# Performance work log

Measured on AMD Instinct MI355X. Metric: run time of the kernel, lower is better.

Reference implementation:

```python
import jax, jax.numpy as jnp
import numpy as np

DIM = 32
ED = DIM * DIM          # 1024
HID = ED * 4            # 4096
EPS = 1e-5


def _ln(x, g, b):
    # LayerNorm over last two dims (d, d)
    m = x.mean(axis=(-2, -1), keepdims=True)
    v = jnp.var(x, axis=(-2, -1), keepdims=True)
    return (x - m) * jax.lax.rsqrt(v + EPS) * g + b


def setup_inputs() -> dict:
    key = jax.random.key(0)
    ks = jax.random.split(key, 10)
    b, s, d = 2, 1024, DIM
    inp = {
        "x": jax.random.normal(ks[0], (b, s, d, d), dtype=jnp.float32),
        # StateSpaceLayer params
        "log_A": jax.random.normal(ks[1], (d,), dtype=jnp.float32) * 0.02,
        "w_dt": jax.random.normal(ks[2], (d,), dtype=jnp.float32) / np.sqrt(d),
        "b_dt": jnp.zeros((), dtype=jnp.float32),
        "g_ssm": jnp.ones((d, d), dtype=jnp.float32),
        "b_ssm": jnp.zeros((d, d), dtype=jnp.float32),
        # FFN params
        "g_ffn": jnp.ones((d, d), dtype=jnp.float32),
        "b_ffn": jnp.zeros((d, d), dtype=jnp.float32),
        "W1": jax.random.normal(ks[3], (ED, HID), dtype=jnp.float32) / np.sqrt(ED),
        "bb1": jnp.zeros((HID,), dtype=jnp.float32),
        "W2": jax.random.normal(ks[4], (HID, ED), dtype=jnp.float32) / np.sqrt(HID),
        "bb2": jnp.zeros((ED,), dtype=jnp.float32),
    }
    return inp


def reference(x, log_A, w_dt, b_dt, g_ssm, b_ssm, g_ffn, b_ffn, W1, bb1, W2, bb2):
    b, s, d, _ = x.shape
    # ---- StateSpaceLayer (parallel / training path) ----
    xn = _ln(x, g_ssm, b_ssm)                          # (b,s,d,d)
    A_cont = -jnp.exp(log_A)                           # (d,)
    # dt_proj: Linear(d,1) over last axis, then squeeze -> (b,s,d)
    dt = jax.nn.softplus(jnp.einsum('bsrc,c->bsr', xn, w_dt) + b_dt)
    log_a = dt * A_cont                                # (b,s,d)
    cs = jnp.cumsum(log_a, axis=1)                     # (b,s,d)
    log_M = cs[:, :, None, :] - cs[:, None, :, :]      # (b,t,j,d)
    tmask = jnp.arange(s)[:, None] >= jnp.arange(s)[None, :]  # (t,j) causal
    M = jnp.where(tmask[None, :, :, None], jnp.exp(log_M), 0.0)
    ssm_out = jnp.einsum('btjr,bjrc->btrc', M, xn) + x  # residual
    # ---- MatrixFeedForward ----
    fn = _ln(ssm_out, g_ffn, b_ffn).reshape(b, s, d * d)
    h = jax.nn.gelu(fn @ W1 + bb1, approximate=False)
    y = (h @ W2 + bb2).reshape(b, s, d, d)
    return ssm_out + y
```

## Files before the change

kernel.cpp:

```cpp
#include <hip/hip_runtime.h>
#include <math.h>

#define EPSF 1e-5f

typedef __attribute__((ext_vector_type(4))) float f32x4;
typedef __attribute__((ext_vector_type(4))) int i32x4;
typedef __attribute__((ext_vector_type(8))) int i32x8;

__device__ __forceinline__ unsigned short f2bf(float f) {
  unsigned int u = __float_as_uint(f);
  u += 0x7FFFu + ((u >> 16) & 1u);
  return (unsigned short)(u >> 16);
}
__device__ __forceinline__ float bf2f(unsigned short u) {
  return __uint_as_float((unsigned int)u << 16);
}

__device__ __forceinline__ void async_load16(const void* g, void* l) {
  __builtin_amdgcn_global_load_lds(
      (const __attribute__((address_space(1))) void*)g,
      (__attribute__((address_space(3))) void*)l, 16, 0, 0);
}


__global__ __launch_bounds__(256) void k_pre(
    const float* __restrict__ x, const float* __restrict__ g, const float* __restrict__ bta,
    const float* __restrict__ w_dt, const float* __restrict__ b_dt,
    const float* __restrict__ log_A, unsigned short* __restrict__ xn, float* __restrict__ log_a,
    const float* __restrict__ W1, unsigned char* __restrict__ W1t,
    const float* __restrict__ W2, unsigned char* __restrict__ W2t) {
  __shared__ float smem[64 * 65];
  int tid = threadIdx.x;
  if (blockIdx.x < 2048) {
    int bs = blockIdx.x;
    int t = tid;
    float4 v = ((const float4*)(x + (size_t)bs * 1024))[t];
    float s = v.x + v.y + v.z + v.w;
    float ss = v.x * v.x + v.y * v.y + v.z * v.z + v.w * v.w;
    #pragma unroll
    for (int o = 1; o < 64; o <<= 1) { s += __shfl_xor(s, o); ss += __shfl_xor(ss, o); }
    float* red = smem;
    int w = t >> 6;
    if ((t & 63) == 0) { red[w] = s; red[4 + w] = ss; }
    __syncthreads();
    float S = red[0] + red[1] + red[2] + red[3];
    float SS = red[4] + red[5] + red[6] + red[7];
    float m = S * (1.0f / 1024.0f);
    float var = SS * (1.0f / 1024.0f) - m * m;
    float inv = rsqrtf(var + EPSF);
    float4 gv = ((const float4*)g)[t];
    float4 bv = ((const float4*)bta)[t];
    float4 o;
    o.x = (v.x - m) * inv * gv.x + bv.x;
    o.y = (v.y - m) * inv * gv.y + bv.y;
    o.z = (v.z - m) * inv * gv.z + bv.z;
    o.w = (v.w - m) * inv * gv.w + bv.w;
    ushort4 ob;
    ob.x = f2bf(o.x); ob.y = f2bf(o.y); ob.z = f2bf(o.z); ob.w = f2bf(o.w);
    ((ushort4*)(xn + (size_t)bs * 1024))[t] = ob;
    float4 wv = ((const float4*)w_dt)[t & 7];
    float part = o.x * wv.x + o.y * wv.y + o.z * wv.z + o.w * wv.w;
    part += __shfl_xor(part, 1);
    part += __shfl_xor(part, 2);
    part += __shfl_xor(part, 4);
    if ((t & 7) == 0) {
      int r = t >> 3;
      float z = part + b_dt[0];
      float sp = (z > 20.0f) ? z : log1pf(expf(z));
      log_a[(size_t)bs * 32 + r] = sp * (-expf(log_A[r]));
    }
  } else {
    int bid = blockIdx.x - 2048;
    bool isW1 = bid < 1024;
    const float* src; unsigned char* dst; int C, r0, c0, NK;
    if (isW1) { src = W1; dst = W1t; C = 4096; NK = 8;
                c0 = (bid & 63) * 64; r0 = (bid >> 6) * 64; }
    else { bid -= 1024; src = W2; dst = W2t; C = 1024; NK = 32;
           c0 = (bid & 15) * 64; r0 = (bid >> 4) * 64; }
    #pragma unroll
    for (int q = 0; q < 4; ++q) {
      int lin = q * 256 + tid;
      int r = lin >> 4, cq = lin & 15;
      float4 v = *(const float4*)(src + (size_t)(r0 + r) * C + c0 + cq * 4);
      smem[r * 65 + cq * 4 + 0] = v.x; smem[r * 65 + cq * 4 + 1] = v.y;
      smem[r * 65 + cq * 4 + 2] = v.z; smem[r * 65 + cq * 4 + 3] = v.w;
    }
    __syncthreads();
    int c = tid & 63, kg = tid >> 6;
    int n = c0 + c;
    int k0 = r0 + kg * 16;
    int pk[4];
    #pragma unroll
    for (int q = 0; q < 4; ++q) {
      int p = __builtin_amdgcn_cvt_pk_fp8_f32(
          smem[(kg * 16 + q * 4 + 0) * 65 + c] * 16.0f,
          smem[(kg * 16 + q * 4 + 1) * 65 + c] * 16.0f, 0, false);
      pk[q] = __builtin_amdgcn_cvt_pk_fp8_f32(
          smem[(kg * 16 + q * 4 + 2) * 65 + c] * 16.0f,
          smem[(kg * 16 + q * 4 + 3) * 65 + c] * 16.0f, p, true);
    }
    size_t sb = (size_t)(n >> 4) * NK + (k0 >> 7);
    int l = ((k0 >> 5) & 3) * 16 + (n & 15);
    int4 o4; o4.x = pk[0]; o4.y = pk[1]; o4.z = pk[2]; o4.w = pk[3];
    *(int4*)(dst + sb * 2048 + ((k0 >> 4) & 1) * 1024 + l * 16) = o4;
  }
}

template <int PASS>
__global__ __launch_bounds__(256) void k_scan_pass(
    const unsigned short* __restrict__ xn, const float* __restrict__ x,
    const float* __restrict__ loga, float4* __restrict__ E, float* __restrict__ P,
    const float* __restrict__ bb2, float* __restrict__ out) {
  int bx = blockIdx.x;
  int b = bx >> 8, r = (bx >> 3) & 31, ch = bx & 7;
  int tid = threadIdx.x, cg = tid & 7, sub = tid >> 3;
  __shared__ float dec[128];
  __shared__ float4 sE[32][8];
  __shared__ float sP[32];
  if (tid < 128)
    dec[tid] = expf(loga[(size_t)(b * 1024 + ch * 128 + tid) * 32 + r]);
  __syncthreads();
  int t0 = ch * 128 + sub * 4;
  size_t base = ((size_t)(b * 1024 + t0) * 1024 + r * 32 + cg * 4) >> 2;
  const ushort4* xn4 = (const ushort4*)xn;
  float4 xv[4];
  #pragma unroll
  for (int i = 0; i < 4; ++i) {
    ushort4 u = xn4[base + (size_t)i * 256];
    xv[i].x = bf2f(u.x); xv[i].y = bf2f(u.y); xv[i].z = bf2f(u.z); xv[i].w = bf2f(u.w);
  }
  float4 S = {0.f, 0.f, 0.f, 0.f};
  float Pl = 1.0f;
  #pragma unroll
  for (int i = 0; i < 4; ++i) {
    float d = dec[sub * 4 + i];
    S.x = d * S.x + xv[i].x; S.y = d * S.y + xv[i].y;
    S.z = d * S.z + xv[i].z; S.w = d * S.w + xv[i].w;
    Pl *= d;
  }
  sE[sub][cg] = S;
  if (cg == 0) sP[sub] = Pl;
  __syncthreads();
  if (PASS == 0) {
    if (tid < 8) {
      float4 Et = {0.f, 0.f, 0.f, 0.f};
      float PP = 1.0f;
      #pragma unroll
      for (int h = 0; h < 32; ++h) {
        float p = sP[h]; float4 e = sE[h][tid];
        Et.x = p * Et.x + e.x; Et.y = p * Et.y + e.y;
        Et.z = p * Et.z + e.z; Et.w = p * Et.w + e.w;
        PP *= p;
      }
      E[((size_t)(b * 32 + r) * 8 + ch) * 8 + tid] = Et;
      if (tid == 0) P[(b * 32 + r) * 8 + ch] = PP;
    }
  } else {
    float4 Sin = {0.f, 0.f, 0.f, 0.f};
    const float4* Eb = E + (size_t)(b * 32 + r) * 64 + cg;
    const float* Pb = P + (size_t)(b * 32 + r) * 8;
    for (int h = 0; h < ch; ++h) {
      float p = Pb[h]; float4 e = Eb[h * 8];
      Sin.x = p * Sin.x + e.x; Sin.y = p * Sin.y + e.y;
      Sin.z = p * Sin.z + e.z; Sin.w = p * Sin.w + e.w;
    }
    for (int h = 0; h < sub; ++h) {
      float p = sP[h]; float4 e = sE[h][cg];
      Sin.x = p * Sin.x + e.x; Sin.y = p * Sin.y + e.y;
      Sin.z = p * Sin.z + e.z; Sin.w = p * Sin.w + e.w;
    }
    float4 bb = ((const float4*)bb2)[r * 8 + cg];
    const float4* x4 = (const float4*)x;
    float4* out4 = (float4*)out;
    #pragma unroll
    for (int i = 0; i < 4; ++i) {
      float d = dec[sub * 4 + i];
      Sin.x = d * Sin.x + xv[i].x; Sin.y = d * Sin.y + xv[i].y;
      Sin.z = d * Sin.z + xv[i].z; Sin.w = d * Sin.w + xv[i].w;
      float4 rx = x4[base + (size_t)i * 256];
      float4 oi;
      oi.x = Sin.x + rx.x + bb.x; oi.y = Sin.y + rx.y + bb.y;
      oi.z = Sin.z + rx.z + bb.z; oi.w = Sin.w + rx.w + bb.w;
      out4[base + (size_t)i * 256] = oi;
    }
  }
}

__global__ __launch_bounds__(256) void k_ln2(
    const float* __restrict__ out, const float* __restrict__ bb2,
    const float* __restrict__ g, const float* __restrict__ bta,
    unsigned char* __restrict__ fn) {
  __shared__ __align__(16) unsigned char sC[16384];
  int tid = threadIdx.x;
  int t15 = tid >> 4;
  int kc = tid & 15;
  int tok = (blockIdx.x << 4) + t15;
  const float4* row = (const float4*)(out + (size_t)tok * 1024);
  const float4* b4 = (const float4*)bb2;
  float4 v[16];
  float s = 0.f, ss = 0.f;
  #pragma unroll
  for (int ci = 0; ci < 4; ++ci) {
    int cc = kc + ci * 16;
    #pragma unroll
    for (int q = 0; q < 4; ++q) {
      float4 xv = row[cc * 4 + q];
      float4 bb = b4[cc * 4 + q];
      xv.x -= bb.x; xv.y -= bb.y; xv.z -= bb.z; xv.w -= bb.w;
      v[ci * 4 + q] = xv;
      s += xv.x + xv.y + xv.z + xv.w;
      ss += xv.x * xv.x + xv.y * xv.y + xv.z * xv.z + xv.w * xv.w;
    }
  }
  #pragma unroll
  for (int o = 1; o < 16; o <<= 1) { s += __shfl_xor(s, o); ss += __shfl_xor(ss, o); }
  float m = s * (1.0f / 1024.0f);
  float var = ss * (1.0f / 1024.0f) - m * m;
  float inv = rsqrtf(var + EPSF);
  #pragma unroll
  for (int ci = 0; ci < 4; ++ci) {
    int cc = kc + ci * 16;
    int pk[4];
    #pragma unroll
    for (int q = 0; q < 4; ++q) {
      float4 gv = ((const float4*)g)[cc * 4 + q];
      float4 bv = ((const float4*)bta)[cc * 4 + q];
      float4 xv = v[ci * 4 + q];
      float f0 = (xv.x - m) * inv * gv.x + bv.x;
      float f1 = (xv.y - m) * inv * gv.y + bv.y;
      float f2 = (xv.z - m) * inv * gv.z + bv.z;
      float f3 = (xv.w - m) * inv * gv.w + bv.w;
      int p = __builtin_amdgcn_cvt_pk_fp8_f32(f0, f1, 0, false);
      pk[q] = __builtin_amdgcn_cvt_pk_fp8_f32(f2, f3, p, true);
    }
    int loc = (cc >> 3) * 2048 + (cc & 1) * 1024 + (((cc >> 1) & 3) * 16 + t15) * 16;
    loc ^= ((loc >> 8) & 7) << 4;
    int4 o4; o4.x = pk[0]; o4.y = pk[1]; o4.z = pk[2]; o4.w = pk[3];
    *(int4*)(sC + loc) = o4;
  }
  __syncthreads();
  unsigned char* dst = fn + (size_t)blockIdx.x * 16384;
  #pragma unroll
  for (int p = 0; p < 4; ++p) {
    int a = (p * 256 + tid) * 16;
    int sa = a ^ (((a >> 8) & 7) << 4);
    *(int4*)(dst + a) = *(const int4*)(sC + sa);
  }
}

__global__ __launch_bounds__(256, 2) void k_gemm1(
    const unsigned char* __restrict__ Ap, const unsigned char* __restrict__ Bp,
    const float* __restrict__ bias, unsigned char* __restrict__ C8) {
  __shared__ __align__(16) unsigned char sAB[65536];
  int L = blockIdx.x;
  int xcd = L & 7;
  int nq = xcd & 3, mh = xcd >> 2;
  int rest = L >> 3;
  int nx = rest & 7, my = rest >> 3;
  int n0 = (nq * 8 + nx) * 128;
  int m0 = (mh * 8 + my) * 128;
  int tid = threadIdx.x;
  int wave = tid >> 6, lane = tid & 63;
  int wr = wave >> 1, wc = wave & 1;
  int l15 = lane & 15, quad = lane >> 4;

  f32x4 zero = {0.0f, 0.0f, 0.0f, 0.0f};
  f32x4 acc[4][4];
  #pragma unroll
  for (int i = 0; i < 4; ++i)
    #pragma unroll
    for (int j = 0; j < 4; ++j) acc[i][j] = zero;

  const unsigned char* gsrc = (wave < 2) ? Ap : Bp;
  int rt0 = (wave < 2) ? (m0 >> 4) : (n0 >> 4);
  int aoff = (wave < 2) ? 0 : 16384;
  int w01 = wave & 1;

  #pragma unroll
  for (int t = 0; t < 8; ++t) {
    int idx = w01 * 8 + t, rt = idx >> 1, h = idx & 1;
    async_load16(gsrc + ((size_t)(rt0 + rt) * 8 + 0) * 2048 + h * 1024 + lane * 16,
                 sAB + aoff + rt * 2048 + h * 1024 + lane * 16);
  }

  #pragma unroll 1
  for (int st = 0; st < 8; ++st) {
    int cur = (st & 1) * 32768;
    if (st < 7) {
      int nxt = cur ^ 32768;
      #pragma unroll
      for (int t = 0; t < 8; ++t) {
        int idx = w01 * 8 + t, rt = idx >> 1, h = idx & 1;
        async_load16(gsrc + ((size_t)(rt0 + rt) * 8 + st + 1) * 2048 + h * 1024 + lane * 16,
                     sAB + nxt + aoff + rt * 2048 + h * 1024 + lane * 16);
      }
      asm volatile("s_waitcnt vmcnt(8)" ::: "memory");
    } else {
      asm volatile("s_waitcnt vmcnt(0)" ::: "memory");
    }
    __builtin_amdgcn_s_barrier();
    const unsigned char* sA = sAB + cur;
    const unsigned char* sB = sAB + cur + 16384;
    i32x8 af[4], bf[4];
    #pragma unroll
    for (int i = 0; i < 4; ++i) {
      const unsigned char* pa = sA + (wr * 4 + i) * 2048 + lane * 16;
      i32x4 lo = *(const i32x4*)pa;
      i32x4 hi = *(const i32x4*)(pa + 1024);
      af[i] = __builtin_shufflevector(lo, hi, 0, 1, 2, 3, 4, 5, 6, 7);
    }
    #pragma unroll
    for (int j = 0; j < 4; ++j) {
      const unsigned char* pb = sB + (wc * 4 + j) * 2048 + lane * 16;
      i32x4 lo = *(const i32x4*)pb;
      i32x4 hi = *(const i32x4*)(pb + 1024);
      bf[j] = __builtin_shufflevector(lo, hi, 0, 1, 2, 3, 4, 5, 6, 7);
    }
    #pragma unroll
    for (int i = 0; i < 4; ++i)
      #pragma unroll
      for (int j = 0; j < 4; ++j)
        acc[i][j] = __builtin_amdgcn_mfma_scale_f32_16x16x128_f8f6f4(
            af[i], bf[j], acc[i][j], 0, 0, 0, 0x7F7F7F7F, 0, 0x7F7F7F7F);
    asm volatile("s_waitcnt lgkmcnt(0)" ::: "memory");
    __builtin_amdgcn_s_barrier();
  }

  unsigned char* sC = sAB;
  #pragma unroll
  for (int i = 0; i < 4; ++i) {
    #pragma unroll
    for (int j = 0; j < 4; ++j) {
      int col_l = wc * 64 + j * 16 + l15;
      float bval = bias[n0 + col_l];
      int half2 = (col_l >> 4) & 1, lb = (col_l >> 5) & 3;
      unsigned char* ld = sC + (wr * 4 + i) * 2048 + half2 * 1024 +
                          (lb * 16 + quad * 4) * 16 + l15;
      float vv[4];
      #pragma unroll
      for (int v = 0; v < 4; ++v) {
        float val = acc[i][j][v] * 0.0625f + bval;
        float u = val * (0.7978845608f + 0.035677408f * val * val);
        vv[v] = val / (1.0f + __expf(-2.0f * u));
      }
      int p01 = __builtin_amdgcn_cvt_pk_fp8_f32(vv[0], vv[1], 0, false);
      int p23 = __builtin_amdgcn_cvt_pk_fp8_f32(vv[2], vv[3], 0, false);
      ld[0 * 16] = (unsigned char)(p01 & 0xff);
      ld[1 * 16] = (unsigned char)((p01 >> 8) & 0xff);
      ld[2 * 16] = (unsigned char)(p23 & 0xff);
      ld[3 * 16] = (unsigned char)((p23 >> 8) & 0xff);
    }
  }
  __syncthreads();
  int mt2_0 = m0 >> 4, kp2 = n0 >> 7;
  #pragma unroll
  for (int p = 0; p < 4; ++p) {
    int ci = p * 256 + tid;
    int s = ci >> 7, off = (ci & 127) * 16;
    *(int4*)(C8 + ((size_t)(mt2_0 + s) * 32 + kp2) * 2048 + off) =
        *(const int4*)(sC + s * 2048 + off);
  }
}

__global__ __launch_bounds__(256, 2) void k_gemm2(
    const unsigned char* __restrict__ Ap, const unsigned char* __restrict__ Bp,
    float* __restrict__ O) {
  __shared__ __align__(16) unsigned char sAB[49152];
  int L = blockIdx.x;
  int n0 = (L & 7) * 128;
  int m0 = (L >> 3) * 64;
  int tid = threadIdx.x;
  int wave = tid >> 6, lane = tid & 63;
  int wr = wave >> 1, wc = wave & 1;
  int l15 = lane & 15, quad = lane >> 4;
  int mt0 = m0 >> 4, nt0 = n0 >> 4;

  f32x4 zero = {0.0f, 0.0f, 0.0f, 0.0f};
  f32x4 acc[2][4];
  #pragma unroll
  for (int i = 0; i < 2; ++i)
    #pragma unroll
    for (int j = 0; j < 4; ++j) acc[i][j] = zero;

  #pragma unroll
  for (int t = 0; t < 6; ++t) {
    int idx = wave * 6 + t;
    if (idx < 8) {
      int rt = idx >> 1, h = idx & 1;
      async_load16(Ap + ((size_t)(mt0 + rt) * 32 + 0) * 2048 + h * 1024 + lane * 16,
                   sAB + rt * 2048 + h * 1024 + lane * 16);
    } else {
      int bh = idx - 8, rt = bh >> 1, h = bh & 1;
      async_load16(Bp + ((size_t)(nt0 + rt) * 32 + 0) * 2048 + h * 1024 + lane * 16,
                   sAB + 8192 + rt * 2048 + h * 1024 + lane * 16);
    }
  }

  #pragma unroll 1
  for (int st = 0; st < 32; ++st) {
    int cur = (st & 1) * 24576;
    if (st < 31) {
      int nxt = cur ^ 24576;
      #pragma unroll
      for (int t = 0; t < 6; ++t) {
        int idx = wave * 6 + t;
        if (idx < 8) {
          int rt = idx >> 1, h = idx & 1;
          async_load16(Ap + ((size_t)(mt0 + rt) * 32 + st + 1) * 2048 + h * 1024 + lane * 16,
                       sAB + nxt + rt * 2048 + h * 1024 + lane * 16);
        } else {
          int bh = idx - 8, rt = bh >> 1, h = bh & 1;
          async_load16(Bp + ((size_t)(nt0 + rt) * 32 + st + 1) * 2048 + h * 1024 + lane * 16,
                       sAB + nxt + 8192 + rt * 2048 + h * 1024 + lane * 16);
        }
      }
      asm volatile("s_waitcnt vmcnt(6)" ::: "memory");
    } else {
      asm volatile("s_waitcnt vmcnt(0)" ::: "memory");
    }
    __builtin_amdgcn_s_barrier();
    const unsigned char* sA = sAB + cur;
    const unsigned char* sB = sAB + cur + 8192;
    i32x8 af[2], bf[4];
    #pragma unroll
    for (int i = 0; i < 2; ++i) {
      const unsigned char* pa = sA + (wr * 2 + i) * 2048 + lane * 16;
      i32x4 lo = *(const i32x4*)pa;
      i32x4 hi = *(const i32x4*)(pa + 1024);
      af[i] = __builtin_shufflevector(lo, hi, 0, 1, 2, 3, 4, 5, 6, 7);
    }
    #pragma unroll
    for (int j = 0; j < 4; ++j) {
      const unsigned char* pb = sB + (wc * 4 + j) * 2048 + lane * 16;
      i32x4 lo = *(const i32x4*)pb;
      i32x4 hi = *(const i32x4*)(pb + 1024);
      bf[j] = __builtin_shufflevector(lo, hi, 0, 1, 2, 3, 4, 5, 6, 7);
    }
    #pragma unroll
    for (int i = 0; i < 2; ++i)
      #pragma unroll
      for (int j = 0; j < 4; ++j)
        acc[i][j] = __builtin_amdgcn_mfma_scale_f32_16x16x128_f8f6f4(
            af[i], bf[j], acc[i][j], 0, 0, 0, 0x7F7F7F7F, 0, 0x7F7F7F7F);
    asm volatile("s_waitcnt lgkmcnt(0)" ::: "memory");
    __builtin_amdgcn_s_barrier();
  }

  #pragma unroll
  for (int i = 0; i < 2; ++i)
    #pragma unroll
    for (int j = 0; j < 4; ++j) {
      int col = n0 + wc * 64 + j * 16 + l15;
      #pragma unroll
      for (int v = 0; v < 4; ++v) {
        int row = m0 + wr * 32 + i * 16 + quad * 4 + v;
        float* p = &O[(size_t)row * 1024 + col];
        *p = *p + acc[i][j][v] * 0.0625f;
      }
    }
}

extern "C" void kernel_launch(void* const* d_in, const int* in_sizes, int n_in,
                              void* d_out, int out_size, void* d_ws, size_t ws_size,
                              hipStream_t stream) {
  const float* x     = (const float*)d_in[0];
  const float* log_A = (const float*)d_in[1];
  const float* w_dt  = (const float*)d_in[2];
  const float* b_dt  = (const float*)d_in[3];
  const float* g_ssm = (const float*)d_in[4];
  const float* b_ssm = (const float*)d_in[5];
  const float* g_ffn = (const float*)d_in[6];
  const float* b_ffn = (const float*)d_in[7];
  const float* W1    = (const float*)d_in[8];
  const float* bb1   = (const float*)d_in[9];
  const float* W2    = (const float*)d_in[10];
  const float* bb2   = (const float*)d_in[11];
  float* out = (float*)d_out;

  const size_t MB = 1u << 20;
  char* ws = (char*)d_ws;
  unsigned short* xn   = (unsigned short*)(ws);
  unsigned char* W1t   = (unsigned char*)(ws + 4 * MB);
  float* loga          = (float*)(ws + 8 * MB);
  float4* Ebuf         = (float4*)(ws + 8 * MB + 262144);
  float* Pbuf          = (float*)(ws + 8 * MB + 393216);
  unsigned char* fn    = (unsigned char*)(ws + 9 * MB);
  unsigned char* W2t   = (unsigned char*)(ws + 11 * MB);
  unsigned char* hbf   = (unsigned char*)(ws + 15 * MB);

  k_pre<<<4096, 256, 0, stream>>>(x, g_ssm, b_ssm, w_dt, b_dt, log_A, xn, loga,
                                  W1, W1t, W2, W2t);
  k_scan_pass<0><<<512, 256, 0, stream>>>(xn, x, loga, Ebuf, Pbuf, bb2, out);
  k_scan_pass<1><<<512, 256, 0, stream>>>(xn, x, loga, Ebuf, Pbuf, bb2, out);
  k_ln2<<<128, 256, 0, stream>>>(out, bb2, g_ffn, b_ffn, fn);
  k_gemm1<<<512, 256, 0, stream>>>(fn, W1t, bb1, hbf);
  k_gemm2<<<256, 256, 0, stream>>>(hbf, W2t, out);
}
```

Before: 155.9 us.

## Move weight FP8 packing into scan passes and retile gemm2 to 64x64 tiles

```diff
diff --git a/kernel.cpp b/kernel.cpp
--- a/kernel.cpp
+++ b/kernel.cpp
@@ -23,65 +23,67 @@
 }
 
 
-__global__ __launch_bounds__(256) void k_pre(
+__global__ __launch_bounds__(256) void k_ln1(
     const float* __restrict__ x, const float* __restrict__ g, const float* __restrict__ bta,
     const float* __restrict__ w_dt, const float* __restrict__ b_dt,
-    const float* __restrict__ log_A, unsigned short* __restrict__ xn, float* __restrict__ log_a,
-    const float* __restrict__ W1, unsigned char* __restrict__ W1t,
-    const float* __restrict__ W2, unsigned char* __restrict__ W2t) {
-  __shared__ float smem[64 * 65];
+    const float* __restrict__ log_A, unsigned short* __restrict__ xn,
+    float* __restrict__ log_a) {
+  __shared__ float red[8];
+  int bs = blockIdx.x;
+  int t = threadIdx.x;
+  float4 v = ((const float4*)(x + (size_t)bs * 1024))[t];
+  float s = v.x + v.y + v.z + v.w;
+  float ss = v.x * v.x + v.y * v.y + v.z * v.z + v.w * v.w;
+  #pragma unroll
+  for (int o = 1; o < 64; o <<= 1) { s += __shfl_xor(s, o); ss += __shfl_xor(ss, o); }
+  int w = t >> 6;
+  if ((t & 63) == 0) { red[w] = s; red[4 + w] = ss; }
+  __syncthreads();
+  float S = red[0] + red[1] + red[2] + red[3];
+  float SS = red[4] + red[5] + red[6] + red[7];
+  float m = S * (1.0f / 1024.0f);
+  float var = SS * (1.0f / 1024.0f) - m * m;
+  float inv = rsqrtf(var + EPSF);
+  float4 gv = ((const float4*)g)[t];
+  float4 bv = ((const float4*)bta)[t];
+  float4 o;
+  o.x = (v.x - m) * inv * gv.x + bv.x;
+  o.y = (v.y - m) * inv * gv.y + bv.y;
+  o.z = (v.z - m) * inv * gv.z + bv.z;
+  o.w = (v.w - m) * inv * gv.w + bv.w;
+  ushort4 ob;
+  ob.x = f2bf(o.x); ob.y = f2bf(o.y); ob.z = f2bf(o.z); ob.w = f2bf(o.w);
+  ((ushort4*)(xn + (size_t)bs * 1024))[t] = ob;
+  float4 wv = ((const float4*)w_dt)[t & 7];
+  float part = o.x * wv.x + o.y * wv.y + o.z * wv.z + o.w * wv.w;
+  part += __shfl_xor(part, 1);
+  part += __shfl_xor(part, 2);
+  part += __shfl_xor(part, 4);
+  if ((t & 7) == 0) {
+    int r = t >> 3;
+    float z = part + b_dt[0];
+    float sp = (z > 20.0f) ? z : log1pf(expf(z));
+    log_a[(size_t)bs * 32 + r] = sp * (-expf(log_A[r]));
+  }
+}
+
+template <int PASS, int NKW>
+__global__ __launch_bounds__(256) void k_scan_pack(
+    const unsigned short* __restrict__ xn, const float* __restrict__ x,
+    const float* __restrict__ loga, float4* __restrict__ E, float* __restrict__ P,
+    const float* __restrict__ bb2, float* __restrict__ out,
+    const float* __restrict__ Wsrc, unsigned char* __restrict__ Wdst, int WC) {
+  __shared__ __align__(16) float smem[64 * 65];
   int tid = threadIdx.x;
-  if (blockIdx.x < 2048) {
-    int bs = blockIdx.x;
-    int t = tid;
-    float4 v = ((const float4*)(x + (size_t)bs * 1024))[t];
-    float s = v.x + v.y + v.z + v.w;
-    float ss = v.x * v.x + v.y * v.y + v.z * v.z + v.w * v.w;
-    #pragma unroll
-    for (int o = 1; o < 64; o <<= 1) { s += __shfl_xor(s, o); ss += __shfl_xor(ss, o); }
-    float* red = smem;
-    int w = t >> 6;
-    if ((t & 63) == 0) { red[w] = s; red[4 + w] = ss; }
-    __syncthreads();
-    float S = red[0] + red[1] + red[2] + red[3];
-    float SS = red[4] + red[5] + red[6] + red[7];
-    float m = S * (1.0f / 1024.0f);
-    float var = SS * (1.0f / 1024.0f) - m * m;
-    float inv = rsqrtf(var + EPSF);
-    float4 gv = ((const float4*)g)[t];
-    float4 bv = ((const float4*)bta)[t];
-    float4 o;
-    o.x = (v.x - m) * inv * gv.x + bv.x;
-    o.y = (v.y - m) * inv * gv.y + bv.y;
-    o.z = (v.z - m) * inv * gv.z + bv.z;
-    o.w = (v.w - m) * inv * gv.w + bv.w;
-    ushort4 ob;
-    ob.x = f2bf(o.x); ob.y = f2bf(o.y); ob.z = f2bf(o.z); ob.w = f2bf(o.w);
-    ((ushort4*)(xn + (size_t)bs * 1024))[t] = ob;
-    float4 wv = ((const float4*)w_dt)[t & 7];
-    float part = o.x * wv.x + o.y * wv.y + o.z * wv.z + o.w * wv.w;
-    part += __shfl_xor(part, 1);
-    part += __shfl_xor(part, 2);
-    part += __shfl_xor(part, 4);
-    if ((t & 7) == 0) {
-      int r = t >> 3;
-      float z = part + b_dt[0];
-      float sp = (z > 20.0f) ? z : log1pf(expf(z));
-      log_a[(size_t)bs * 32 + r] = sp * (-expf(log_A[r]));
-    }
-  } else {
-    int bid = blockIdx.x - 2048;
-    bool isW1 = bid < 1024;
-    const float* src; unsigned char* dst; int C, r0, c0, NK;
-    if (isW1) { src = W1; dst = W1t; C = 4096; NK = 8;
-                c0 = (bid & 63) * 64; r0 = (bid >> 6) * 64; }
-    else { bid -= 1024; src = W2; dst = W2t; C = 1024; NK = 32;
-           c0 = (bid & 15) * 64; r0 = (bid >> 4) * 64; }
+  if (blockIdx.x >= 512) {
+    int bid = blockIdx.x - 512;
+    int ncg = WC >> 6;
+    int c0 = (bid % ncg) * 64, r0 = (bid / ncg) * 64;
     #pragma unroll
     for (int q = 0; q < 4; ++q) {
       int lin = q * 256 + tid;
       int r = lin >> 4, cq = lin & 15;
-      float4 v = *(const float4*)(src + (size_t)(r0 + r) * C + c0 + cq * 4);
+      float4 v = *(const float4*)(Wsrc + (size_t)(r0 + r) * WC + c0 + cq * 4);
       smem[r * 65 + cq * 4 + 0] = v.x; smem[r * 65 + cq * 4 + 1] = v.y;
       smem[r * 65 + cq * 4 + 2] = v.z; smem[r * 65 + cq * 4 + 3] = v.w;
     }
@@ -99,24 +101,18 @@
           smem[(kg * 16 + q * 4 + 2) * 65 + c] * 16.0f,
           smem[(kg * 16 + q * 4 + 3) * 65 + c] * 16.0f, p, true);
     }
-    size_t sb = (size_t)(n >> 4) * NK + (k0 >> 7);
+    size_t sb = (size_t)(n >> 4) * NKW + (k0 >> 7);
     int l = ((k0 >> 5) & 3) * 16 + (n & 15);
     int4 o4; o4.x = pk[0]; o4.y = pk[1]; o4.z = pk[2]; o4.w = pk[3];
-    *(int4*)(dst + sb * 2048 + ((k0 >> 4) & 1) * 1024 + l * 16) = o4;
-  }
-}
-
-template <int PASS>
-__global__ __launch_bounds__(256) void k_scan_pass(
-    const unsigned short* __restrict__ xn, const float* __restrict__ x,
-    const float* __restrict__ loga, float4* __restrict__ E, float* __restrict__ P,
-    const float* __restrict__ bb2, float* __restrict__ out) {
+    *(int4*)(Wdst + sb * 2048 + ((k0 >> 4) & 1) * 1024 + l * 16) = o4;
+    return;
+  }
+  float* dec = smem;
+  float4* sE = (float4*)(smem + 128);
+  float* sP = smem + 128 + 1024;
   int bx = blockIdx.x;
   int b = bx >> 8, r = (bx >> 3) & 31, ch = bx & 7;
-  int tid = threadIdx.x, cg = tid & 7, sub = tid >> 3;
-  __shared__ float dec[128];
-  __shared__ float4 sE[32][8];
-  __shared__ float sP[32];
+  int cg = tid & 7, sub = tid >> 3;
   if (tid < 128)
     dec[tid] = expf(loga[(size_t)(b * 1024 + ch * 128 + tid) * 32 + r]);
   __syncthreads();
@@ -138,7 +134,7 @@
     S.z = d * S.z + xv[i].z; S.w = d * S.w + xv[i].w;
     Pl *= d;
   }
-  sE[sub][cg] = S;
+  sE[sub * 8 + cg] = S;
   if (cg == 0) sP[sub] = Pl;
   __syncthreads();
   if (PASS == 0) {
@@ -147,7 +143,7 @@
       float PP = 1.0f;
       #pragma unroll
       for (int h = 0; h < 32; ++h) {
-        float p = sP[h]; float4 e = sE[h][tid];
+        float p = sP[h]; float4 e = sE[h * 8 + tid];
         Et.x = p * Et.x + e.x; Et.y = p * Et.y + e.y;
         Et.z = p * Et.z + e.z; Et.w = p * Et.w + e.w;
         PP *= p;
@@ -165,7 +161,7 @@
       Sin.z = p * Sin.z + e.z; Sin.w = p * Sin.w + e.w;
     }
     for (int h = 0; h < sub; ++h) {
-      float p = sP[h]; float4 e = sE[h][cg];
+      float p = sP[h]; float4 e = sE[h * 8 + cg];
       Sin.x = p * Sin.x + e.x; Sin.y = p * Sin.y + e.y;
       Sin.z = p * Sin.z + e.z; Sin.w = p * Sin.w + e.w;
     }
@@ -365,83 +361,83 @@
 __global__ __launch_bounds__(256, 2) void k_gemm2(
     const unsigned char* __restrict__ Ap, const unsigned char* __restrict__ Bp,
     float* __restrict__ O) {
-  __shared__ __align__(16) unsigned char sAB[49152];
+  __shared__ __align__(16) unsigned char sAB[65536];
   int L = blockIdx.x;
-  int n0 = (L & 7) * 128;
-  int m0 = (L >> 3) * 64;
+  int xcd = L & 7;
+  int mq = xcd >> 1, nh = xcd & 1;
+  int rest = L >> 3;
+  int nx = rest & 7, my = rest >> 3;
+  int n0 = (nh * 8 + nx) * 64;
+  int m0 = (mq * 8 + my) * 64;
   int tid = threadIdx.x;
   int wave = tid >> 6, lane = tid & 63;
   int wr = wave >> 1, wc = wave & 1;
   int l15 = lane & 15, quad = lane >> 4;
-  int mt0 = m0 >> 4, nt0 = n0 >> 4;
 
   f32x4 zero = {0.0f, 0.0f, 0.0f, 0.0f};
-  f32x4 acc[2][4];
+  f32x4 acc[2][2];
   #pragma unroll
   for (int i = 0; i < 2; ++i)
     #pragma unroll
-    for (int j = 0; j < 4; ++j) acc[i][j] = zero;
-
-  #pragma unroll
-  for (int t = 0; t < 6; ++t) {
-    int idx = wave * 6 + t;
-    if (idx < 8) {
-      int rt = idx >> 1, h = idx & 1;
-      async_load16(Ap + ((size_t)(mt0 + rt) * 32 + 0) * 2048 + h * 1024 + lane * 16,
-                   sAB + rt * 2048 + h * 1024 + lane * 16);
-    } else {
-      int bh = idx - 8, rt = bh >> 1, h = bh & 1;
-      async_load16(Bp + ((size_t)(nt0 + rt) * 32 + 0) * 2048 + h * 1024 + lane * 16,
-                   sAB + 8192 + rt * 2048 + h * 1024 + lane * 16);
-    }
+    for (int j = 0; j < 2; ++j) acc[i][j] = zero;
+
+  const unsigned char* gsrc = (wave < 2) ? Ap : Bp;
+  int rt0 = (wave < 2) ? (m0 >> 4) : (n0 >> 4);
+  int aoff = (wave < 2) ? 0 : 16384;
+  int w01 = wave & 1;
+
+  #pragma unroll
+  for (int t = 0; t < 8; ++t) {
+    int idx = w01 * 8 + t, sb = idx >> 1, h = idx & 1;
+    int rt = sb >> 1, kt = sb & 1;
+    async_load16(gsrc + ((size_t)(rt0 + rt) * 32 + kt) * 2048 + h * 1024 + lane * 16,
+                 sAB + aoff + sb * 2048 + h * 1024 + lane * 16);
   }
 
   #pragma unroll 1
-  for (int st = 0; st < 32; ++st) {
-    int cur = (st & 1) * 24576;
-    if (st < 31) {
-      int nxt = cur ^ 24576;
-      #pragma unroll
-      for (int t = 0; t < 6; ++t) {
-        int idx = wave * 6 + t;
-        if (idx < 8) {
-          int rt = idx >> 1, h = idx & 1;
-          async_load16(Ap + ((size_t)(mt0 + rt) * 32 + st + 1) * 2048 + h * 1024 + lane * 16,
-                       sAB + nxt + rt * 2048 + h * 1024 + lane * 16);
-        } else {
-          int bh = idx - 8, rt = bh >> 1, h = bh & 1;
-          async_load16(Bp + ((size_t)(nt0 + rt) * 32 + st + 1) * 2048 + h * 1024 + lane * 16,
-                       sAB + nxt + 8192 + rt * 2048 + h * 1024 + lane * 16);
-        }
-      }
-      asm volatile("s_waitcnt vmcnt(6)" ::: "memory");
+  for (int st = 0; st < 16; ++st) {
+    int cur = (st & 1) * 32768;
+    if (st < 15) {
+      int nxt = cur ^ 32768;
+      #pragma unroll
+      for (int t = 0; t < 8; ++t) {
+        int idx = w01 * 8 + t, sb = idx >> 1, h = idx & 1;
+        int rt = sb >> 1, kt = sb & 1;
+        async_load16(
+            gsrc + ((size_t)(rt0 + rt) * 32 + (st + 1) * 2 + kt) * 2048 + h * 1024 + lane * 16,
+            sAB + nxt + aoff + sb * 2048 + h * 1024 + lane * 16);
+      }
+      asm volatile("s_waitcnt vmcnt(8)" ::: "memory");
     } else {
       asm volatile("s_waitcnt vmcnt(0)" ::: "memory");
     }
     __builtin_amdgcn_s_barrier();
     const unsigned char* sA = sAB + cur;
-    const unsigned char* sB = sAB + cur + 8192;
-    i32x8 af[2], bf[4];
-    #pragma unroll
-    for (int i = 0; i < 2; ++i) {
-      const unsigned char* pa = sA + (wr * 2 + i) * 2048 + lane * 16;
-      i32x4 lo = *(const i32x4*)pa;
-      i32x4 hi = *(const i32x4*)(pa + 1024);
-      af[i] = __builtin_shufflevector(lo, hi, 0, 1, 2, 3, 4, 5, 6, 7);
-    }
-    #pragma unroll
-    for (int j = 0; j < 4; ++j) {
-      const unsigned char* pb = sB + (wc * 4 + j) * 2048 + lane * 16;
-      i32x4 lo = *(const i32x4*)pb;
-      i32x4 hi = *(const i32x4*)(pb + 1024);
-      bf[j] = __builtin_shufflevector(lo, hi, 0, 1, 2, 3, 4, 5, 6, 7);
-    }
-    #pragma unroll
-    for (int i = 0; i < 2; ++i)
-      #pragma unroll
-      for (int j = 0; j < 4; ++j)
-        acc[i][j] = __builtin_amdgcn_mfma_scale_f32_16x16x128_f8f6f4(
-            af[i], bf[j], acc[i][j], 0, 0, 0, 0x7F7F7F7F, 0, 0x7F7F7F7F);
+    const unsigned char* sB = sAB + cur + 16384;
+    #pragma unroll
+    for (int kl = 0; kl < 2; ++kl) {
+      i32x8 af[2], bf[2];
+      #pragma unroll
+      for (int i = 0; i < 2; ++i) {
+        const unsigned char* pa = sA + ((wr * 2 + i) * 2 + kl) * 2048 + lane * 16;
+        i32x4 lo = *(const i32x4*)pa;
+        i32x4 hi = *(const i32x4*)(pa + 1024);
+        af[i] = __builtin_shufflevector(lo, hi, 0, 1, 2, 3, 4, 5, 6, 7);
+      }
+      #pragma unroll
+      for (int j = 0; j < 2; ++j) {
+        const unsigned char* pb = sB + ((wc * 2 + j) * 2 + kl) * 2048 + lane * 16;
+        i32x4 lo = *(const i32x4*)pb;
+        i32x4 hi = *(const i32x4*)(pb + 1024);
+        bf[j] = __builtin_shufflevector(lo, hi, 0, 1, 2, 3, 4, 5, 6, 7);
+      }
+      #pragma unroll
+      for (int i = 0; i < 2; ++i)
+        #pragma unroll
+        for (int j = 0; j < 2; ++j)
+          acc[i][j] = __builtin_amdgcn_mfma_scale_f32_16x16x128_f8f6f4(
+              af[i], bf[j], acc[i][j], 0, 0, 0, 0x7F7F7F7F, 0, 0x7F7F7F7F);
+    }
     asm volatile("s_waitcnt lgkmcnt(0)" ::: "memory");
     __builtin_amdgcn_s_barrier();
   }
@@ -449,8 +445,8 @@
   #pragma unroll
   for (int i = 0; i < 2; ++i)
     #pragma unroll
-    for (int j = 0; j < 4; ++j) {
-      int col = n0 + wc * 64 + j * 16 + l15;
+    for (int j = 0; j < 2; ++j) {
+      int col = n0 + wc * 32 + j * 16 + l15;
       #pragma unroll
       for (int v = 0; v < 4; ++v) {
         int row = m0 + wr * 32 + i * 16 + quad * 4 + v;
@@ -488,11 +484,12 @@
   unsigned char* W2t   = (unsigned char*)(ws + 11 * MB);
   unsigned char* hbf   = (unsigned char*)(ws + 15 * MB);
 
-  k_pre<<<4096, 256, 0, stream>>>(x, g_ssm, b_ssm, w_dt, b_dt, log_A, xn, loga,
-                                  W1, W1t, W2, W2t);
-  k_scan_pass<0><<<512, 256, 0, stream>>>(xn, x, loga, Ebuf, Pbuf, bb2, out);
-  k_scan_pass<1><<<512, 256, 0, stream>>>(xn, x, loga, Ebuf, Pbuf, bb2, out);
+  k_ln1<<<2048, 256, 0, stream>>>(x, g_ssm, b_ssm, w_dt, b_dt, log_A, xn, loga);
+  k_scan_pack<0, 8><<<1536, 256, 0, stream>>>(xn, x, loga, Ebuf, Pbuf, bb2, out,
+                                              W1, W1t, 4096);
+  k_scan_pack<1, 32><<<1536, 256, 0, stream>>>(xn, x, loga, Ebuf, Pbuf, bb2, out,
+                                               W2, W2t, 1024);
   k_ln2<<<128, 256, 0, stream>>>(out, bb2, g_ffn, b_ffn, fn);
   k_gemm1<<<512, 256, 0, stream>>>(fn, W1t, bb1, hbf);
-  k_gemm2<<<256, 256, 0, stream>>>(hbf, W2t, out);
-}
+  k_gemm2<<<512, 256, 0, stream>>>(hbf, W2t, out);
+}
```

Measured after the change: 149.0 us. -4.5%, faster.
